# Kernel optimization log

Hardware: AMD Instinct MI355X
Metric: run time of the kernel (lower is better)

## Reference

```python
import jax, jax.numpy as jnp
import numpy as np

B, S, D = 2, 2048, 2048
H = 16
Q_LORA, KV_LORA = 1536, 512
D_NOPE, D_ROPE, D_V = 128, 64, 128
QK_D = D_NOPE + D_ROPE  # 192
EPS = 1e-6
ROPE_THETA = 10000.0


def rms_norm(x, w, eps=EPS):
    return x * jax.lax.rsqrt(jnp.mean(x * x, axis=-1, keepdims=True) + eps) * w


def apply_rope(x, cos, sin):
    # x: [b, s, h, d]; cos/sin: [s, d//2]; pairs are interleaved (x0,x1),(x2,x3),...
    xr, xi = x[..., 0::2], x[..., 1::2]
    c = cos[None, :, None, :]
    s = sin[None, :, None, :]
    yr = xr * c - xi * s
    yi = xr * s + xi * c
    return jnp.stack([yr, yi], axis=-1).reshape(x.shape)


def setup_inputs() -> dict:
    key = jax.random.key(0)
    ks = jax.random.split(key, 8)
    sd = 0.02
    pos = jnp.arange(S, dtype=jnp.float32)
    inv_freq = 1.0 / (ROPE_THETA ** (jnp.arange(0, D_ROPE, 2, dtype=jnp.float32) / D_ROPE))
    ang = pos[:, None] * inv_freq[None, :]  # [S, D_ROPE//2]
    mask = jnp.triu(jnp.full((S, S), float('-inf'), dtype=jnp.float32), k=1)
    return {
        'x': jax.random.normal(ks[0], (B, S, D), dtype=jnp.float32),
        'freqs_cos': jnp.cos(ang),
        'freqs_sin': jnp.sin(ang),
        'mask': mask,
        'wq_a': jax.random.normal(ks[1], (Q_LORA, D), dtype=jnp.float32) * sd,
        'q_norm_w': jnp.ones((Q_LORA,), dtype=jnp.float32),
        'wq_b': jax.random.normal(ks[2], (H * QK_D, Q_LORA), dtype=jnp.float32) * sd,
        'wkv_a': jax.random.normal(ks[3], (KV_LORA + D_ROPE, D), dtype=jnp.float32) * sd,
        'kv_norm_w': jnp.ones((KV_LORA,), dtype=jnp.float32),
        'wkv_b': jax.random.normal(ks[4], (H * (D_NOPE + D_V), KV_LORA), dtype=jnp.float32) * sd,
        'wo': jax.random.normal(ks[5], (D, H * D_V), dtype=jnp.float32) * sd,
    }


def reference(x, freqs_cos, freqs_sin, mask, wq_a, q_norm_w, wq_b, wkv_a, kv_norm_w, wkv_b, wo):
    b, s, _ = x.shape
    # query path: down-proj -> RMSNorm -> up-proj
    q = rms_norm(x @ wq_a.T, q_norm_w) @ wq_b.T          # [b, s, H*QK_D]
    q = q.reshape(b, s, H, QK_D)
    q_nope, q_pe = q[..., :D_NOPE], q[..., D_NOPE:]
    q_pe = apply_rope(q_pe, freqs_cos, freqs_sin)
    # kv path: joint down-proj, split latent / rope key
    kv_full = x @ wkv_a.T                                 # [b, s, KV_LORA + D_ROPE]
    kv, k_pe = kv_full[..., :KV_LORA], kv_full[..., KV_LORA:]
    k_pe = apply_rope(k_pe[:, :, None, :], freqs_cos, freqs_sin)  # [b, s, 1, D_ROPE]
    q = jnp.concatenate([q_nope, q_pe], axis=-1)          # [b, s, H, QK_D]
    kv = rms_norm(kv, kv_norm_w) @ wkv_b.T                # [b, s, H*(D_NOPE+D_V)]
    kv = kv.reshape(b, s, H, D_NOPE + D_V)
    k_nope, v = kv[..., :D_NOPE], kv[..., D_NOPE:]
    k = jnp.concatenate([k_nope, jnp.broadcast_to(k_pe, (b, s, H, D_ROPE))], axis=-1)
    scale = QK_D ** -0.5
    scores = jnp.einsum('bshd,bthd->bsht', q, k) * scale + mask[None, :, None, :]
    probs = jax.nn.softmax(scores.astype(jnp.float32), axis=-1).astype(x.dtype)
    out = jnp.einsum('bsht,bthd->bshd', probs, v).reshape(b, s, H * D_V)
    return out @ wo.T
```

## Files before the change

kernel.cpp:

```cpp
#include <hip/hip_runtime.h>
#include <hip/hip_bf16.h>

typedef __bf16 bf16_t;
typedef __bf16 bf16x8 __attribute__((ext_vector_type(8)));
typedef __bf16 bf16x4 __attribute__((ext_vector_type(4)));
typedef float  f32x4  __attribute__((ext_vector_type(4)));

#define NB 2
#define NS 2048
#define ND 2048
#define NH 16
#define QLORA 1536
#define KVLORA 512
#define DNOPE 128
#define DROPE 64
#define DVDIM 128
#define QKD 192

#define QSCALE 0.10411754f

#if __has_builtin(__builtin_amdgcn_exp2f)
#define EXP2F(x) __builtin_amdgcn_exp2f(x)
#else
#define EXP2F(x) __expf((x) * 0.69314718056f)
#endif
#if __has_builtin(__builtin_amdgcn_rcpf)
#define RCPF(x) __builtin_amdgcn_rcpf(x)
#else
#define RCPF(x) (1.0f / (x))
#endif

typedef __attribute__((address_space(3))) void as3_void;
typedef __attribute__((address_space(1))) const void as1_void;
__device__ __forceinline__ void gload16(const void* g, void* l) {
  __builtin_amdgcn_global_load_lds((as1_void*)g, (as3_void*)l, 16, 0, 0);
}

__global__ __launch_bounds__(256) void k_cvt_all(
    const float* __restrict__ x, const float* __restrict__ wqa,
    const float* __restrict__ wqb, const float* __restrict__ wkva,
    const float* __restrict__ wkvb, const float* __restrict__ wo,
    bf16_t* __restrict__ xb, bf16_t* __restrict__ wqab, bf16_t* __restrict__ wqbb,
    bf16_t* __restrict__ wkvab, bf16_t* __restrict__ wkvbb, bf16_t* __restrict__ wob) {
  const int c0 = 2097152, c1 = 2883584, c2 = 4063232, c3 = 4358144, c4 = 4882432,
            c5 = 5931008;
  int i = blockIdx.x * 256 + threadIdx.x;
  for (; i < c5; i += gridDim.x * 256) {
    const float* src;
    bf16_t* dst;
    int off;
    if (i < c0) { src = x; dst = xb; off = i; }
    else if (i < c1) { src = wqa; dst = wqab; off = i - c0; }
    else if (i < c2) { src = wqb; dst = wqbb; off = i - c1; }
    else if (i < c3) { src = wkva; dst = wkvab; off = i - c2; }
    else if (i < c4) { src = wkvb; dst = wkvbb; off = i - c3; }
    else { src = wo; dst = wob; off = i - c4; }
    float4 v = reinterpret_cast<const float4*>(src)[off];
    bf16x4 o = {(bf16_t)v.x, (bf16_t)v.y, (bf16_t)v.z, (bf16_t)v.w};
    reinterpret_cast<bf16x4*>(dst)[off] = o;
  }
}

template <int EPI>
__global__ __launch_bounds__(256) void k_gemm_bt(
    const bf16_t* __restrict__ A, const bf16_t* __restrict__ Bw,
    float* __restrict__ Cf, float* __restrict__ Cf2,
    bf16_t* __restrict__ Kout, bf16_t* __restrict__ Vtout,
    const float* __restrict__ fc, const float* __restrict__ fs,
    int M, int N, int K) {
  __shared__ bf16_t As[2][128 * 64];
  __shared__ bf16_t Bs[2][128 * 64];
  const int tid = threadIdx.x;
  const int lane = tid & 63;
  const int wave = tid >> 6;
  const int wm = (wave >> 1) * 64, wn = (wave & 1) * 64;
  const int m0 = blockIdx.y * 128, n0 = blockIdx.x * 128;
  const int l15 = lane & 15, l4 = lane >> 4;
  const int srow = lane >> 3;
  const int scol = ((lane & 7) ^ srow) * 8;

  const f32x4 Z4 = {0.f, 0.f, 0.f, 0.f};
  f32x4 acc[4][4];
#pragma unroll
  for (int i = 0; i < 4; ++i)
#pragma unroll
    for (int j = 0; j < 4; ++j) acc[i][j] = Z4;

  auto stage = [&](int buf, int k0) {
#pragma unroll
    for (int c = 0; c < 4; ++c) {
      int chunk = c * 4 + wave;
      int row = chunk * 8 + srow;
      gload16(A + (size_t)(m0 + row) * K + k0 + scol, &As[buf][chunk * 512]);
      gload16(Bw + (size_t)(n0 + row) * K + k0 + scol, &Bs[buf][chunk * 512]);
    }
  };

  const int nk = K >> 6;
  stage(0, 0);
  __syncthreads();
  int cur = 0;
#pragma unroll 1
  for (int t = 0; t < nk; ++t) {
    if (t + 1 < nk) stage(cur ^ 1, (t + 1) * 64);
#pragma unroll
    for (int ks = 0; ks < 2; ++ks) {
      int kc = ks * 4 + l4;
      int pc = (kc ^ (l15 & 7)) * 8;
      bf16x8 af[4], bfr[4];
#pragma unroll
      for (int f = 0; f < 4; ++f) {
        af[f] = *reinterpret_cast<const bf16x8*>(&As[cur][(wm + f * 16 + l15) * 64 + pc]);
        bfr[f] = *reinterpret_cast<const bf16x8*>(&Bs[cur][(wn + f * 16 + l15) * 64 + pc]);
      }
#pragma unroll
      for (int fi = 0; fi < 4; ++fi)
#pragma unroll
        for (int fj = 0; fj < 4; ++fj)
          acc[fi][fj] = __builtin_amdgcn_mfma_f32_16x16x32_bf16(af[fi], bfr[fj], acc[fi][fj], 0, 0, 0);
    }
    __syncthreads();
    cur ^= 1;
  }

#pragma unroll
  for (int fi = 0; fi < 4; ++fi) {
#pragma unroll
    for (int fj = 0; fj < 4; ++fj) {
      int col = n0 + wn + fj * 16 + l15;
#pragma unroll
      for (int r = 0; r < 4; ++r) {
        int row = m0 + wm + fi * 16 + l4 * 4 + r;
        float v = acc[fi][fj][r];
        if (EPI == 0) {
          if (col < N) Cf[(size_t)row * N + col] = v;
        } else if (EPI == 1) {
          int h = col >> 8, rr = col & 255;
          int b = row >> 11, s = row & 2047;
          if (rr < DNOPE)
            Kout[(((size_t)(b * NH + h)) * NS + s) * QKD + rr] = (bf16_t)v;
          else
            Vtout[(((size_t)(b * NH + h)) * DVDIM + (rr - DNOPE)) * NS + s] = (bf16_t)v;
        } else if (EPI == 2) {
          int h = col / 192;
          int d = col - h * 192;
          int b = row >> 11, s = row & 2047;
          float y = v;
          if (d >= DNOPE) {
            float pv = __shfl_xor(v, 1);
            int pp = ((d & ~1) - DNOPE) >> 1;
            float c = fc[s * 32 + pp], si = fs[s * 32 + pp];
            y = (col & 1) ? (pv * si + v * c) : (v * c - pv * si);
          }
          Kout[((size_t)(b * NH + h) * NS + s) * QKD + d] = (bf16_t)(y * QSCALE);
        } else {
          if (col < QLORA) Cf[(size_t)row * QLORA + col] = v;
          else if (col < QLORA + KVLORA + DROPE)
            Cf2[(size_t)row * (KVLORA + DROPE) + (col - QLORA)] = v;
        }
      }
    }
  }
}

template <int COLS>
__global__ __launch_bounds__(256) void k_rmsnorm(const float* __restrict__ in,
                                                 const float* __restrict__ w,
                                                 bf16_t* __restrict__ out) {
  int row = blockIdx.x;
  const float* rp = in + (size_t)row * COLS;
  float ss = 0.f;
  for (int c = threadIdx.x * 4; c < COLS; c += 1024) {
    float4 v = *reinterpret_cast<const float4*>(rp + c);
    ss += v.x * v.x + v.y * v.y + v.z * v.z + v.w * v.w;
  }
#pragma unroll
  for (int m = 32; m; m >>= 1) ss += __shfl_xor(ss, m);
  __shared__ float red[4];
  if ((threadIdx.x & 63) == 0) red[threadIdx.x >> 6] = ss;
  __syncthreads();
  float tot = red[0] + red[1] + red[2] + red[3];
  float rs = rsqrtf(tot / (float)COLS + 1e-6f);
  for (int c = threadIdx.x * 4; c < COLS; c += 1024) {
    float4 v = *reinterpret_cast<const float4*>(rp + c);
    bf16x4 o = {(bf16_t)(v.x * rs * w[c]), (bf16_t)(v.y * rs * w[c + 1]),
                (bf16_t)(v.z * rs * w[c + 2]), (bf16_t)(v.w * rs * w[c + 3])};
    *reinterpret_cast<bf16x4*>(out + (size_t)row * COLS + c) = o;
  }
}

__global__ __launch_bounds__(256) void k_kv_post(const float* __restrict__ kvf,
                                                 const float* __restrict__ w,
                                                 const float* __restrict__ fc,
                                                 const float* __restrict__ fs,
                                                 bf16_t* __restrict__ kvn,
                                                 bf16_t* __restrict__ Kb) {
  int row = blockIdx.x;
  const float* rp = kvf + (size_t)row * (KVLORA + DROPE);
  float ss = 0.f;
  float4 v = {0.f, 0.f, 0.f, 0.f};
  if (threadIdx.x < 128) {
    v = reinterpret_cast<const float4*>(rp)[threadIdx.x];
    ss = v.x * v.x + v.y * v.y + v.z * v.z + v.w * v.w;
  }
#pragma unroll
  for (int m = 32; m; m >>= 1) ss += __shfl_xor(ss, m);
  __shared__ float red[4];
  if ((threadIdx.x & 63) == 0) red[threadIdx.x >> 6] = ss;
  __syncthreads();
  float tot = red[0] + red[1] + red[2] + red[3];
  float rs = rsqrtf(tot / (float)KVLORA + 1e-6f);
  if (threadIdx.x < 128) {
    int c = threadIdx.x * 4;
    bf16x4 o = {(bf16_t)(v.x * rs * w[c]), (bf16_t)(v.y * rs * w[c + 1]),
                (bf16_t)(v.z * rs * w[c + 2]), (bf16_t)(v.w * rs * w[c + 3])};
    *reinterpret_cast<bf16x4*>(kvn + (size_t)row * KVLORA + c) = o;
  }
  int b = row >> 11, s = row & 2047;
  if (threadIdx.x < 32) {
    int p = threadIdx.x;
    float x0 = rp[KVLORA + 2 * p], x1 = rp[KVLORA + 2 * p + 1];
    float c = fc[s * 32 + p], si = fs[s * 32 + p];
    float yr = x0 * c - x1 * si, yi = x0 * si + x1 * c;
    bf16_t br = (bf16_t)yr, bi = (bf16_t)yi;
    for (int h = 0; h < NH; ++h) {
      size_t ob = ((size_t)(b * NH + h) * NS + s) * QKD + DNOPE;
      Kb[ob + 2 * p] = br;
      Kb[ob + 2 * p + 1] = bi;
    }
  }
}

__global__ __launch_bounds__(512) void k_attn(const bf16_t* __restrict__ Qb,
                                              const bf16_t* __restrict__ Kb,
                                              const bf16_t* __restrict__ Vtb,
                                              bf16_t* __restrict__ Ao) {
  __shared__ bf16x8 Ks[64 * 24];
  __shared__ bf16x8 Vs[128 * 8];
  __shared__ bf16x8 Ps[8 * 16 * 8];
  const int id = blockIdx.x;
  const int s_ = id >> 3;
  const int bh = (id & 7) + 8 * (s_ & 3);
  const int bx = s_ >> 2;
  const int b = bh >> 4, h = bh & 15;
  const int tid = threadIdx.x;
  const int lane = tid & 63, wave = tid >> 6;
  const int l15 = lane & 15, l4 = lane >> 4;
  const size_t bhNS = (size_t)bh * NS;
  const size_t bhDV = (size_t)bh * DVDIM;
  bf16_t* Pw = reinterpret_cast<bf16_t*>(&Ps[wave * 128]);
  const f32x4 Z4 = {0.f, 0.f, 0.f, 0.f};

  int krow[3], kkc[3], vrw[2], vkc[2];
#pragma unroll
  for (int i = 0; i < 3; ++i) {
    int c = tid + i * 512;
    krow[i] = c / 24;
    kkc[i] = c - krow[i] * 24;
  }
#pragma unroll
  for (int i = 0; i < 2; ++i) {
    int c = tid + i * 512;
    vrw[i] = c >> 3;
    vkc[i] = c & 7;
  }

#pragma unroll 1
  for (int phase = 0; phase < 2; ++phase) {
    const int qt = (phase == 0) ? (15 - bx) : bx;
    const int q0 = qt * 128;
    const int qrow = q0 + wave * 16;
    const int ntiles = 2 * qt + 2;

    bf16x8 qf[6];
    {
      const bf16_t* qrp = Qb + (bhNS + qrow + l15) * QKD;
#pragma unroll
      for (int kc = 0; kc < 6; ++kc)
        qf[kc] = reinterpret_cast<const bf16x8*>(qrp)[kc * 4 + l4];
    }

    f32x4 oacc[8];
#pragma unroll
    for (int i = 0; i < 8; ++i) oacc[i] = Z4;
    float mrun[4], lrun[4];
#pragma unroll
    for (int r = 0; r < 4; ++r) {
      mrun[r] = -3e38f;
      lrun[r] = 0.f;
    }

    bf16x8 kpre[3], vpre[2];
#pragma unroll
    for (int i = 0; i < 3; ++i)
      kpre[i] = reinterpret_cast<const bf16x8*>(Kb + (bhNS + krow[i]) * QKD)[kkc[i]];
#pragma unroll
    for (int i = 0; i < 2; ++i)
      vpre[i] = reinterpret_cast<const bf16x8*>(Vtb + (bhDV + vrw[i]) * NS)[vkc[i]];

#pragma unroll 1
    for (int kt = 0; kt < ntiles; ++kt) {
      const int kv0 = kt * 64;
      __builtin_amdgcn_sched_barrier(0);
      __builtin_amdgcn_s_barrier();
#pragma unroll
      for (int i = 0; i < 3; ++i)
        Ks[krow[i] * 24 + ((kkc[i] & ~7) | ((kkc[i] ^ krow[i]) & 7))] = kpre[i];
#pragma unroll
      for (int i = 0; i < 2; ++i)
        Vs[vrw[i] * 8 + (vkc[i] ^ (vrw[i] & 7))] = vpre[i];
      if (kt + 1 < ntiles) {
        const int nk = kv0 + 64;
#pragma unroll
        for (int i = 0; i < 3; ++i)
          kpre[i] = reinterpret_cast<const bf16x8*>(Kb + (bhNS + nk + krow[i]) * QKD)[kkc[i]];
#pragma unroll
        for (int i = 0; i < 2; ++i)
          vpre[i] = reinterpret_cast<const bf16x8*>(Vtb + (bhDV + vrw[i]) * NS + nk)[vkc[i]];
      }
      __builtin_amdgcn_sched_barrier(0);
      asm volatile("s_waitcnt lgkmcnt(0)" ::: "memory");
      __builtin_amdgcn_s_barrier();
      __builtin_amdgcn_sched_barrier(0);

      if (qrow + 15 >= kv0) {
        f32x4 sacc[4];
#pragma unroll
        for (int sub = 0; sub < 4; ++sub) {
          sacc[sub] = Z4;
#pragma unroll
          for (int ksc = 0; ksc < 6; ++ksc) {
            int row = sub * 16 + l15;
            int kc = ksc * 4 + l4;
            bf16x8 kf = Ks[row * 24 + ((kc & ~7) | ((kc ^ row) & 7))];
            sacc[sub] = __builtin_amdgcn_mfma_f32_16x16x32_bf16(qf[ksc], kf, sacc[sub], 0, 0, 0);
          }
        }

        float sbuf[4][4];
        float mloc[4] = {-3e38f, -3e38f, -3e38f, -3e38f};
        const bool msk = (kv0 >= q0);
#pragma unroll
        for (int sub = 0; sub < 4; ++sub) {
#pragma unroll
          for (int r = 0; r < 4; ++r) {
            float s = sacc[sub][r];
            if (msk) {
              int colg = kv0 + sub * 16 + l15;
              int rowg = qrow + l4 * 4 + r;
              if (colg > rowg) s = -3e38f;
            }
            sbuf[sub][r] = s;
            mloc[r] = fmaxf(mloc[r], s);
          }
        }
#pragma unroll
        for (int m = 1; m < 16; m <<= 1)
#pragma unroll
          for (int r = 0; r < 4; ++r) mloc[r] = fmaxf(mloc[r], __shfl_xor(mloc[r], m));

        float d0 = fmaxf(fmaxf(mloc[0] - mrun[0], mloc[1] - mrun[1]),
                         fmaxf(mloc[2] - mrun[2], mloc[3] - mrun[3]));
        if (!__all(d0 <= 0.f)) {
#pragma unroll
          for (int r = 0; r < 4; ++r) {
            float mn = fmaxf(mrun[r], mloc[r]);
            float fac = EXP2F(mrun[r] - mn);
            mrun[r] = mn;
            lrun[r] *= fac;
#pragma unroll
            for (int dc = 0; dc < 8; ++dc) oacc[dc][r] *= fac;
          }
        }

        float rsum[4] = {0.f, 0.f, 0.f, 0.f};
#pragma unroll
        for (int sub = 0; sub < 4; ++sub) {
#pragma unroll
          for (int r = 0; r < 4; ++r) {
            float p = EXP2F(sbuf[sub][r] - mrun[r]);
            rsum[r] += p;
            int prow = l4 * 4 + r;
            int pcol = sub * 16 + l15;
            Pw[prow * 64 + (((pcol >> 3) ^ (prow & 7)) << 3) + (pcol & 7)] = (bf16_t)p;
          }
        }
#pragma unroll
        for (int m = 1; m < 16; m <<= 1)
#pragma unroll
          for (int r = 0; r < 4; ++r) rsum[r] += __shfl_xor(rsum[r], m);
#pragma unroll
        for (int r = 0; r < 4; ++r) lrun[r] += rsum[r];

#pragma unroll
        for (int ks = 0; ks < 2; ++ks) {
          int kc = ks * 4 + l4;
          bf16x8 paf = reinterpret_cast<bf16x8*>(Pw)[l15 * 8 + (kc ^ (l15 & 7))];
#pragma unroll
          for (int dc = 0; dc < 8; ++dc) {
            int vrow = dc * 16 + l15;
            bf16x8 vf = Vs[vrow * 8 + (kc ^ (vrow & 7))];
            oacc[dc] = __builtin_amdgcn_mfma_f32_16x16x32_bf16(paf, vf, oacc[dc], 0, 0, 0);
          }
        }
      }
    }

#pragma unroll
    for (int r = 0; r < 4; ++r) lrun[r] = RCPF(lrun[r]);
#pragma unroll
    for (int dc = 0; dc < 8; ++dc) {
      int dv = dc * 16 + l15;
#pragma unroll
      for (int r = 0; r < 4; ++r) {
        int rowg = qrow + l4 * 4 + r;
        float v = oacc[dc][r] * lrun[r];
        Ao[((size_t)(b * NS + rowg)) * (NH * DVDIM) + h * DVDIM + dv] = (bf16_t)v;
      }
    }
  }
}

extern "C" void kernel_launch(void* const* d_in, const int* in_sizes, int n_in,
                              void* d_out, int out_size, void* d_ws, size_t ws_size,
                              hipStream_t stream) {
  (void)in_sizes; (void)n_in; (void)out_size; (void)ws_size;
  const float* x = (const float*)d_in[0];
  const float* fcos = (const float*)d_in[1];
  const float* fsin = (const float*)d_in[2];
  const float* wq_a = (const float*)d_in[4];
  const float* q_norm_w = (const float*)d_in[5];
  const float* wq_b = (const float*)d_in[6];
  const float* wkv_a = (const float*)d_in[7];
  const float* kv_norm_w = (const float*)d_in[8];
  const float* wkv_b = (const float*)d_in[9];
  const float* wo = (const float*)d_in[10];
  float* out = (float*)d_out;

  char* p = (char*)d_ws;
  bf16_t* x_bf = (bf16_t*)(p);
  bf16_t* wqa_bf = (bf16_t*)(p + 16777216);
  bf16_t* wkva_bf = (bf16_t*)(p + 23068672);
  bf16_t* wqb_bf = (bf16_t*)(p + 25427968);
  bf16_t* wkvb_bf = (bf16_t*)(p + 34865152);
  bf16_t* wo_bf = (bf16_t*)(p + 39059456);
  float* qa_f32 = (float*)(p + 47448064);
  bf16_t* Kb = (bf16_t*)(p + 47448064);
  bf16_t* qan_bf = (bf16_t*)(p + 72613888);
  bf16_t* Qb = (bf16_t*)(p + 85196800);
  char* r2 = p + 110362624;
  float* kvf_f32 = (float*)(r2);
  bf16_t* kvn_bf = (bf16_t*)(r2 + 9437184);
  bf16_t* Vtb = (bf16_t*)(r2 + 13631488);
  bf16_t* attn_bf = (bf16_t*)(r2 + 30408704);

  k_cvt_all<<<2048, 256, 0, stream>>>(x, wq_a, wq_b, wkv_a, wkv_b, wo, x_bf, wqa_bf,
                                      wqb_bf, wkva_bf, wkvb_bf, wo_bf);

  k_gemm_bt<3><<<dim3(17, 32), 256, 0, stream>>>(x_bf, wqa_bf, qa_f32, kvf_f32,
                                                 nullptr, nullptr, nullptr, nullptr,
                                                 NB * NS, QLORA + KVLORA + DROPE, ND);
  k_rmsnorm<QLORA><<<NB * NS, 256, 0, stream>>>(qa_f32, q_norm_w, qan_bf);
  k_kv_post<<<NB * NS, 256, 0, stream>>>(kvf_f32, kv_norm_w, fcos, fsin, kvn_bf, Kb);
  k_gemm_bt<2><<<dim3(24, 32), 256, 0, stream>>>(qan_bf, wqb_bf, nullptr, nullptr, Qb,
                                                 nullptr, fcos, fsin, NB * NS, NH * QKD,
                                                 QLORA);
  k_gemm_bt<1><<<dim3(32, 32), 256, 0, stream>>>(kvn_bf, wkvb_bf, nullptr, nullptr, Kb,
                                                 Vtb, nullptr, nullptr, NB * NS,
                                                 NH * (DNOPE + DVDIM), KVLORA);
  k_attn<<<dim3(256), 512, 0, stream>>>(Qb, Kb, Vtb, attn_bf);
  k_gemm_bt<0><<<dim3(16, 32), 256, 0, stream>>>(attn_bf, wo_bf, out, nullptr, nullptr,
                                                 nullptr, nullptr, nullptr, NB * NS, ND,
                                                 NH * DVDIM);
}
```

Measured before the change: 367.4 us.

## Rewrite attention with 32x32 MFMA, register-resident P, one q-tile per block

The attention kernel moves from 16x16x32 to 32x32x16 bf16 MFMAs, computing S^T so each lane owns one query row. Row max and row sum then need only a single cross-half shuffle. The P matrix is packed to bf16 in registers and exchanged between the two lane halves with shuffles instead of being staged through LDS. The launch changes from 256 blocks of 512 threads, each handling a paired long and short q-tile, to 512 blocks of 256 threads, each handling one q-tile, with the long tiles scheduled first. This cuts LDS traffic and shuffle reductions, but raises register pressure and the per-block work becomes more imbalanced.

```diff
diff --git a/kernel.cpp b/kernel.cpp
--- a/kernel.cpp
+++ b/kernel.cpp
@@ -4,7 +4,9 @@
 typedef __bf16 bf16_t;
 typedef __bf16 bf16x8 __attribute__((ext_vector_type(8)));
 typedef __bf16 bf16x4 __attribute__((ext_vector_type(4)));
+typedef __bf16 bf16x2 __attribute__((ext_vector_type(2)));
 typedef float  f32x4  __attribute__((ext_vector_type(4)));
+typedef float  f32x16 __attribute__((ext_vector_type(16)));
 
 #define NB 2
 #define NS 2048
@@ -34,6 +36,11 @@
 typedef __attribute__((address_space(1))) const void as1_void;
 __device__ __forceinline__ void gload16(const void* g, void* l) {
   __builtin_amdgcn_global_load_lds((as1_void*)g, (as3_void*)l, 16, 0, 0);
+}
+
+__device__ __forceinline__ int pack2(float a, float b) {
+  bf16x2 t = {(bf16_t)a, (bf16_t)b};
+  return __builtin_bit_cast(int, t);
 }
 
 __global__ __launch_bounds__(256) void k_cvt_all(
@@ -231,194 +238,189 @@
   }
 }
 
-__global__ __launch_bounds__(512) void k_attn(const bf16_t* __restrict__ Qb,
+__global__ __launch_bounds__(256) void k_attn(const bf16_t* __restrict__ Qb,
                                               const bf16_t* __restrict__ Kb,
                                               const bf16_t* __restrict__ Vtb,
                                               bf16_t* __restrict__ Ao) {
-  __shared__ bf16x8 Ks[64 * 24];
-  __shared__ bf16x8 Vs[128 * 8];
-  __shared__ bf16x8 Ps[8 * 16 * 8];
+  __shared__ bf16x8 Ks8[64 * 24];
+  __shared__ bf16x8 Vs8[128 * 8];
   const int id = blockIdx.x;
-  const int s_ = id >> 3;
-  const int bh = (id & 7) + 8 * (s_ & 3);
-  const int bx = s_ >> 2;
+  const int bh = id & 31;
+  const int aa = (id >> 5) & 7;
+  const int qt = (id >> 8) ? aa : (15 - aa);
   const int b = bh >> 4, h = bh & 15;
   const int tid = threadIdx.x;
   const int lane = tid & 63, wave = tid >> 6;
-  const int l15 = lane & 15, l4 = lane >> 4;
+  const int l31 = lane & 31, hi = lane >> 5;
+  const int q0w = qt * 128 + wave * 32;
+  const int qg = q0w + l31;
+  const int c4 = hi * 4;
+  const int ntiles = 2 * qt + 2;
   const size_t bhNS = (size_t)bh * NS;
-  const size_t bhDV = (size_t)bh * DVDIM;
-  bf16_t* Pw = reinterpret_cast<bf16_t*>(&Ps[wave * 128]);
-  const f32x4 Z4 = {0.f, 0.f, 0.f, 0.f};
-
-  int krow[3], kkc[3], vrw[2], vkc[2];
-#pragma unroll
-  for (int i = 0; i < 3; ++i) {
-    int c = tid + i * 512;
-    krow[i] = c / 24;
-    kkc[i] = c - krow[i] * 24;
-  }
-#pragma unroll
-  for (int i = 0; i < 2; ++i) {
-    int c = tid + i * 512;
-    vrw[i] = c >> 3;
-    vkc[i] = c & 7;
-  }
+
+  const bf16_t* kptr[6];
+  const bf16_t* vptr[4];
+#pragma unroll
+  for (int i = 0; i < 6; ++i) {
+    int p = tid + i * 256;
+    int row = p / 24, pc = p % 24;
+    int lc = (pc & ~7) | ((pc ^ row) & 7);
+    kptr[i] = Kb + (bhNS + row) * QKD + lc * 8;
+  }
+#pragma unroll
+  for (int i = 0; i < 4; ++i) {
+    int p = tid + i * 256;
+    int row = p >> 3, pc = p & 7;
+    int lc = pc ^ (row & 7);
+    vptr[i] = Vtb + ((size_t)bh * DVDIM + row) * NS + lc * 8;
+  }
+
+  bf16x8 qf[12];
+  {
+    const bf16_t* qp = Qb + (bhNS + qg) * QKD + hi * 8;
+#pragma unroll
+    for (int ks = 0; ks < 12; ++ks)
+      qf[ks] = *reinterpret_cast<const bf16x8*>(qp + ks * 16);
+  }
+
+  f32x16 oacc[4];
+#pragma unroll
+  for (int d = 0; d < 4; ++d) oacc[d] = {};
+  float mrun = -3e38f, lrun = 0.f;
+
+  bf16x8 kpre[6], vpre[4];
+#pragma unroll
+  for (int i = 0; i < 6; ++i) kpre[i] = *reinterpret_cast<const bf16x8*>(kptr[i]);
+#pragma unroll
+  for (int i = 0; i < 4; ++i) vpre[i] = *reinterpret_cast<const bf16x8*>(vptr[i]);
 
 #pragma unroll 1
-  for (int phase = 0; phase < 2; ++phase) {
-    const int qt = (phase == 0) ? (15 - bx) : bx;
-    const int q0 = qt * 128;
-    const int qrow = q0 + wave * 16;
-    const int ntiles = 2 * qt + 2;
-
-    bf16x8 qf[6];
-    {
-      const bf16_t* qrp = Qb + (bhNS + qrow + l15) * QKD;
-#pragma unroll
-      for (int kc = 0; kc < 6; ++kc)
-        qf[kc] = reinterpret_cast<const bf16x8*>(qrp)[kc * 4 + l4];
-    }
-
-    f32x4 oacc[8];
-#pragma unroll
-    for (int i = 0; i < 8; ++i) oacc[i] = Z4;
-    float mrun[4], lrun[4];
-#pragma unroll
-    for (int r = 0; r < 4; ++r) {
-      mrun[r] = -3e38f;
-      lrun[r] = 0.f;
-    }
-
-    bf16x8 kpre[3], vpre[2];
-#pragma unroll
-    for (int i = 0; i < 3; ++i)
-      kpre[i] = reinterpret_cast<const bf16x8*>(Kb + (bhNS + krow[i]) * QKD)[kkc[i]];
-#pragma unroll
-    for (int i = 0; i < 2; ++i)
-      vpre[i] = reinterpret_cast<const bf16x8*>(Vtb + (bhDV + vrw[i]) * NS)[vkc[i]];
-
-#pragma unroll 1
-    for (int kt = 0; kt < ntiles; ++kt) {
-      const int kv0 = kt * 64;
-      __builtin_amdgcn_sched_barrier(0);
-      __builtin_amdgcn_s_barrier();
-#pragma unroll
-      for (int i = 0; i < 3; ++i)
-        Ks[krow[i] * 24 + ((kkc[i] & ~7) | ((kkc[i] ^ krow[i]) & 7))] = kpre[i];
-#pragma unroll
-      for (int i = 0; i < 2; ++i)
-        Vs[vrw[i] * 8 + (vkc[i] ^ (vrw[i] & 7))] = vpre[i];
-      if (kt + 1 < ntiles) {
-        const int nk = kv0 + 64;
-#pragma unroll
-        for (int i = 0; i < 3; ++i)
-          kpre[i] = reinterpret_cast<const bf16x8*>(Kb + (bhNS + nk + krow[i]) * QKD)[kkc[i]];
-#pragma unroll
-        for (int i = 0; i < 2; ++i)
-          vpre[i] = reinterpret_cast<const bf16x8*>(Vtb + (bhDV + vrw[i]) * NS + nk)[vkc[i]];
-      }
-      __builtin_amdgcn_sched_barrier(0);
-      asm volatile("s_waitcnt lgkmcnt(0)" ::: "memory");
-      __builtin_amdgcn_s_barrier();
-      __builtin_amdgcn_sched_barrier(0);
-
-      if (qrow + 15 >= kv0) {
-        f32x4 sacc[4];
-#pragma unroll
-        for (int sub = 0; sub < 4; ++sub) {
-          sacc[sub] = Z4;
-#pragma unroll
-          for (int ksc = 0; ksc < 6; ++ksc) {
-            int row = sub * 16 + l15;
-            int kc = ksc * 4 + l4;
-            bf16x8 kf = Ks[row * 24 + ((kc & ~7) | ((kc ^ row) & 7))];
-            sacc[sub] = __builtin_amdgcn_mfma_f32_16x16x32_bf16(qf[ksc], kf, sacc[sub], 0, 0, 0);
-          }
+  for (int kt = 0; kt < ntiles; ++kt) {
+    const int kv0 = kt * 64;
+    __builtin_amdgcn_s_barrier();
+#pragma unroll
+    for (int i = 0; i < 6; ++i) Ks8[tid + i * 256] = kpre[i];
+#pragma unroll
+    for (int i = 0; i < 4; ++i) Vs8[tid + i * 256] = vpre[i];
+    if (kt + 1 < ntiles) {
+#pragma unroll
+      for (int i = 0; i < 6; ++i) {
+        kptr[i] += 64 * QKD;
+        kpre[i] = *reinterpret_cast<const bf16x8*>(kptr[i]);
+      }
+#pragma unroll
+      for (int i = 0; i < 4; ++i) {
+        vptr[i] += 64;
+        vpre[i] = *reinterpret_cast<const bf16x8*>(vptr[i]);
+      }
+    }
+    __builtin_amdgcn_sched_barrier(0);
+    asm volatile("s_waitcnt lgkmcnt(0)" ::: "memory");
+    __builtin_amdgcn_s_barrier();
+    __builtin_amdgcn_sched_barrier(0);
+
+    if (kv0 > q0w + 31) continue;
+
+    f32x16 sacc[2];
+    sacc[0] = {};
+    sacc[1] = {};
+#pragma unroll
+    for (int ks = 0; ks < 12; ++ks) {
+#pragma unroll
+      for (int kh = 0; kh < 2; ++kh) {
+        int row = kh * 32 + l31;
+        int c = ks * 2 + hi;
+        int pc = (c & ~7) | ((c ^ row) & 7);
+        sacc[kh] = __builtin_amdgcn_mfma_f32_32x32x16_bf16(Ks8[row * 24 + pc], qf[ks],
+                                                           sacc[kh], 0, 0, 0);
+      }
+    }
+
+    const bool diag = (kv0 + 63 > q0w);
+    float mloc = -3e38f;
+#pragma unroll
+    for (int kh = 0; kh < 2; ++kh)
+#pragma unroll
+      for (int rg = 0; rg < 16; ++rg) {
+        float s = sacc[kh][rg];
+        if (diag) {
+          int kg = kv0 + kh * 32 + (rg & 3) + 8 * (rg >> 2) + c4;
+          if (kg > qg) s = -3e38f;
+          sacc[kh][rg] = s;
         }
-
-        float sbuf[4][4];
-        float mloc[4] = {-3e38f, -3e38f, -3e38f, -3e38f};
-        const bool msk = (kv0 >= q0);
-#pragma unroll
-        for (int sub = 0; sub < 4; ++sub) {
-#pragma unroll
-          for (int r = 0; r < 4; ++r) {
-            float s = sacc[sub][r];
-            if (msk) {
-              int colg = kv0 + sub * 16 + l15;
-              int rowg = qrow + l4 * 4 + r;
-              if (colg > rowg) s = -3e38f;
-            }
-            sbuf[sub][r] = s;
-            mloc[r] = fmaxf(mloc[r], s);
-          }
-        }
-#pragma unroll
-        for (int m = 1; m < 16; m <<= 1)
-#pragma unroll
-          for (int r = 0; r < 4; ++r) mloc[r] = fmaxf(mloc[r], __shfl_xor(mloc[r], m));
-
-        float d0 = fmaxf(fmaxf(mloc[0] - mrun[0], mloc[1] - mrun[1]),
-                         fmaxf(mloc[2] - mrun[2], mloc[3] - mrun[3]));
-        if (!__all(d0 <= 0.f)) {
-#pragma unroll
-          for (int r = 0; r < 4; ++r) {
-            float mn = fmaxf(mrun[r], mloc[r]);
-            float fac = EXP2F(mrun[r] - mn);
-            mrun[r] = mn;
-            lrun[r] *= fac;
-#pragma unroll
-            for (int dc = 0; dc < 8; ++dc) oacc[dc][r] *= fac;
-          }
-        }
-
-        float rsum[4] = {0.f, 0.f, 0.f, 0.f};
-#pragma unroll
-        for (int sub = 0; sub < 4; ++sub) {
-#pragma unroll
-          for (int r = 0; r < 4; ++r) {
-            float p = EXP2F(sbuf[sub][r] - mrun[r]);
-            rsum[r] += p;
-            int prow = l4 * 4 + r;
-            int pcol = sub * 16 + l15;
-            Pw[prow * 64 + (((pcol >> 3) ^ (prow & 7)) << 3) + (pcol & 7)] = (bf16_t)p;
-          }
-        }
-#pragma unroll
-        for (int m = 1; m < 16; m <<= 1)
-#pragma unroll
-          for (int r = 0; r < 4; ++r) rsum[r] += __shfl_xor(rsum[r], m);
-#pragma unroll
-        for (int r = 0; r < 4; ++r) lrun[r] += rsum[r];
-
-#pragma unroll
-        for (int ks = 0; ks < 2; ++ks) {
-          int kc = ks * 4 + l4;
-          bf16x8 paf = reinterpret_cast<bf16x8*>(Pw)[l15 * 8 + (kc ^ (l15 & 7))];
-#pragma unroll
-          for (int dc = 0; dc < 8; ++dc) {
-            int vrow = dc * 16 + l15;
-            bf16x8 vf = Vs[vrow * 8 + (kc ^ (vrow & 7))];
-            oacc[dc] = __builtin_amdgcn_mfma_f32_16x16x32_bf16(paf, vf, oacc[dc], 0, 0, 0);
-          }
-        }
-      }
-    }
-
-#pragma unroll
-    for (int r = 0; r < 4; ++r) lrun[r] = RCPF(lrun[r]);
-#pragma unroll
-    for (int dc = 0; dc < 8; ++dc) {
-      int dv = dc * 16 + l15;
-#pragma unroll
-      for (int r = 0; r < 4; ++r) {
-        int rowg = qrow + l4 * 4 + r;
-        float v = oacc[dc][r] * lrun[r];
-        Ao[((size_t)(b * NS + rowg)) * (NH * DVDIM) + h * DVDIM + dv] = (bf16_t)v;
-      }
-    }
-  }
+        mloc = fmaxf(mloc, s);
+      }
+    mloc = fmaxf(mloc, __shfl_xor(mloc, 32));
+
+    if (!__all(mloc <= mrun)) {
+      float mn = fmaxf(mrun, mloc);
+      float fac = EXP2F(mrun - mn);
+      mrun = mn;
+      lrun *= fac;
+#pragma unroll
+      for (int d = 0; d < 4; ++d)
+#pragma unroll
+        for (int rg = 0; rg < 16; ++rg) oacc[d][rg] *= fac;
+    }
+
+    float rsum = 0.f;
+    int W[8][2];
+#pragma unroll
+    for (int kh = 0; kh < 2; ++kh)
+#pragma unroll
+      for (int g = 0; g < 4; ++g) {
+        float p0 = EXP2F(sacc[kh][4 * g + 0] - mrun);
+        float p1 = EXP2F(sacc[kh][4 * g + 1] - mrun);
+        float p2 = EXP2F(sacc[kh][4 * g + 2] - mrun);
+        float p3 = EXP2F(sacc[kh][4 * g + 3] - mrun);
+        rsum += (p0 + p1) + (p2 + p3);
+        W[kh * 4 + g][0] = pack2(p0, p1);
+        W[kh * 4 + g][1] = pack2(p2, p3);
+      }
+    rsum += __shfl_xor(rsum, 32);
+    lrun += rsum;
+
+    bf16x8 pa[4];
+#pragma unroll
+    for (int pks = 0; pks < 4; ++pks) {
+      int kh = pks >> 1, G0 = (pks & 1) * 2;
+      int a0 = W[kh * 4 + G0][0], a1 = W[kh * 4 + G0][1];
+      int b0 = W[kh * 4 + G0 + 1][0], b1 = W[kh * 4 + G0 + 1][1];
+      int own0 = hi ? b0 : a0, own1 = hi ? b1 : a1;
+      int oth0 = hi ? a0 : b0, oth1 = hi ? a1 : b1;
+      int rc0 = __shfl_xor(oth0, 32), rc1 = __shfl_xor(oth1, 32);
+      int4 wv;
+      wv.x = hi ? rc0 : own0;
+      wv.y = hi ? rc1 : own1;
+      wv.z = hi ? own0 : rc0;
+      wv.w = hi ? own1 : rc1;
+      pa[pks] = __builtin_bit_cast(bf16x8, wv);
+    }
+
+#pragma unroll
+    for (int pks = 0; pks < 4; ++pks)
+#pragma unroll
+      for (int dvt = 0; dvt < 4; ++dvt) {
+        int row = dvt * 32 + l31;
+        int pc = (pks * 2 + hi) ^ (row & 7);
+        oacc[dvt] = __builtin_amdgcn_mfma_f32_32x32x16_bf16(Vs8[row * 8 + pc], pa[pks],
+                                                            oacc[dvt], 0, 0, 0);
+      }
+  }
+
+  float lr = RCPF(lrun);
+  bf16_t* base = Ao + ((size_t)(b * NS) + qg) * (NH * DVDIM) + h * DVDIM;
+#pragma unroll
+  for (int dvt = 0; dvt < 4; ++dvt)
+#pragma unroll
+    for (int rg4 = 0; rg4 < 4; ++rg4) {
+      int dv0 = dvt * 32 + 8 * rg4 + c4;
+      bf16x4 o = {(bf16_t)(oacc[dvt][rg4 * 4 + 0] * lr),
+                  (bf16_t)(oacc[dvt][rg4 * 4 + 1] * lr),
+                  (bf16_t)(oacc[dvt][rg4 * 4 + 2] * lr),
+                  (bf16_t)(oacc[dvt][rg4 * 4 + 3] * lr)};
+      *reinterpret_cast<bf16x4*>(base + dv0) = o;
+    }
 }
 
 extern "C" void kernel_launch(void* const* d_in, const int* in_sizes, int n_in,
@@ -468,7 +470,7 @@
   k_gemm_bt<1><<<dim3(32, 32), 256, 0, stream>>>(kvn_bf, wkvb_bf, nullptr, nullptr, Kb,
                                                  Vtb, nullptr, nullptr, NB * NS,
                                                  NH * (DNOPE + DVDIM), KVLORA);
-  k_attn<<<dim3(256), 512, 0, stream>>>(Qb, Kb, Vtb, attn_bf);
+  k_attn<<<dim3(512), 256, 0, stream>>>(Qb, Kb, Vtb, attn_bf);
   k_gemm_bt<0><<<dim3(16, 32), 256, 0, stream>>>(attn_bf, wo_bf, out, nullptr, nullptr,
                                                  nullptr, nullptr, nullptr, NB * NS, ND,
                                                  NH * DVDIM);
```

Result: slower. 405.5 us (+10.4%).
